# Kernel tuning notes

Measured on AMD Instinct MI355X. Metric: run time of the kernel, lower is better.

## Reference

```python
import jax, jax.numpy as jnp
import numpy as np
import math

B, T, C = 2, 2048, 1024
H = 16
D = C // H

def setup_inputs() -> dict:
    key = jax.random.key(0)
    k1, k2, k3, k4, k5 = jax.random.split(key, 5)
    scale = 0.02
    return {
        "x": jax.random.normal(k1, (B, T, C), dtype=jnp.float32),
        "w_attn": jax.random.normal(k2, (3 * C, C), dtype=jnp.float32) * scale,
        "b_attn": jax.random.normal(k3, (3 * C,), dtype=jnp.float32) * scale,
        "w_proj": jax.random.normal(k4, (C, C), dtype=jnp.float32) * scale,
        "b_proj": jax.random.normal(k5, (C,), dtype=jnp.float32) * scale,
    }

def reference(x, w_attn, b_attn, w_proj, b_proj):
    b, t, c = x.shape
    # c_attn: torch Linear -> x @ W.T + b, output [b, t, 3c]
    qkv = jnp.einsum('btc,fc->btf', x, w_attn) + b_attn
    # einops 'b t (a h d) -> a b h t d' with a=3, h=H
    qkv = qkv.reshape(b, t, 3, H, D).transpose(2, 0, 3, 1, 4)
    q, k, v = qkv[0], qkv[1], qkv[2]  # each [b, h, t, d]
    att = jnp.einsum('bhtd,bhsd->bhts', q, k) * (1.0 / math.sqrt(D))
    # causal mask: positions s > t are masked
    mask = jnp.tril(jnp.ones((t, t), dtype=bool))
    att = jnp.where(mask[None, None, :, :], att, jnp.float32(-jnp.inf))
    att = jax.nn.softmax(att, axis=-1)
    y = jnp.einsum('bhts,bhsd->bhtd', att, v)  # [b, h, t, d]
    y = y.transpose(0, 2, 1, 3).reshape(b, t, c)
    return jnp.einsum('btc,fc->btf', y, w_proj) + b_proj
```

## Files before the change

kernel.cpp:

```cpp
#include <hip/hip_runtime.h>
#include <hip/hip_bf16.h>
#include <stdint.h>

typedef unsigned short u16;
typedef __attribute__((ext_vector_type(8))) __bf16 bvec8;
typedef __attribute__((ext_vector_type(4))) float f32x4;
typedef __attribute__((ext_vector_type(16))) float f32x16;

__device__ __forceinline__ u16 f32_to_bf16(float f) {
    uint32_t u = __float_as_uint(f);
    u += 0x7fffu + ((u >> 16) & 1u);
    return (u16)(u >> 16);
}
__device__ __forceinline__ uint32_t pack_bf16x2(float lo, float hi) {
    union { __hip_bfloat162 h; uint32_t u; } c;
    c.h = __float22bfloat162_rn(make_float2(lo, hi));
    return c.u;
}

__device__ __forceinline__ void gl2lds16(const u16* g, u16* l) {
    void* gnc = const_cast<void*>((const void*)g);
    __builtin_amdgcn_global_load_lds(
        (__attribute__((address_space(1))) uint32_t*)gnc,
        (__attribute__((address_space(3))) uint32_t*)((void*)l),
        16, 0, 0);
}

__global__ __launch_bounds__(256) void cvt3(
    const float* __restrict__ a, int na4, const float* __restrict__ b, int nb4,
    const float* __restrict__ c, int nc4,
    u16* __restrict__ oa, u16* __restrict__ ob, u16* __restrict__ oc)
{
    int i = blockIdx.x * 256 + threadIdx.x;
    const float* src; u16* dst; int off;
    if (i < na4)             { src = a; dst = oa; off = i; }
    else if (i < na4 + nb4)  { src = b; dst = ob; off = i - na4; }
    else if (i < na4 + nb4 + nc4) { src = c; dst = oc; off = i - na4 - nb4; }
    else return;
    float4 v = ((const float4*)src)[off];
    ushort4 o;
    o.x = f32_to_bf16(v.x); o.y = f32_to_bf16(v.y);
    o.z = f32_to_bf16(v.z); o.w = f32_to_bf16(v.w);
    ((ushort4*)dst)[off] = o;
}

template <int BNt, bool OUT_BF16>
__global__ __launch_bounds__(256) void gemm_bt_bias(
    const u16* __restrict__ A, const u16* __restrict__ B,
    const float* __restrict__ bias, void* __restrict__ Cv,
    int M, int N, int K)
{
    constexpr int NT = BNt / 32;
    __shared__ __attribute__((aligned(16))) u16 As[128 * 32];
    __shared__ __attribute__((aligned(16))) u16 Bs[BNt * 32];

    const int tid = threadIdx.x, wave = tid >> 6, lane = tid & 63;
    const int col = lane & 15, quad = lane >> 4;
    const int m0 = blockIdx.y * 128, n0 = blockIdx.x * BNt;
    const int wm = (wave >> 1) * 64, wn = (wave & 1) * (BNt / 2);
    const int srow = lane >> 2, schunk = lane & 3;
    const u16* Ag = A + (size_t)(m0 + wave * 32) * K;

    f32x4 acc[4][NT];
#pragma unroll
    for (int i = 0; i < 4; i++)
#pragma unroll
        for (int j = 0; j < NT; j++) acc[i][j] = f32x4{0.f, 0.f, 0.f, 0.f};

    for (int k0 = 0; k0 < K; k0 += 32) {
        __syncthreads();
        gl2lds16(Ag + (size_t)(srow)      * K + k0 + schunk * 8, &As[(wave * 2 + 0) * 512]);
        gl2lds16(Ag + (size_t)(16 + srow) * K + k0 + schunk * 8, &As[(wave * 2 + 1) * 512]);
        if constexpr (BNt == 128) {
            const u16* Bg = B + (size_t)(n0 + wave * 32) * K;
            gl2lds16(Bg + (size_t)(srow)      * K + k0 + schunk * 8, &Bs[(wave * 2 + 0) * 512]);
            gl2lds16(Bg + (size_t)(16 + srow) * K + k0 + schunk * 8, &Bs[(wave * 2 + 1) * 512]);
        } else {
            const u16* Bg = B + (size_t)(n0 + wave * 16) * K;
            gl2lds16(Bg + (size_t)(srow)      * K + k0 + schunk * 8, &Bs[wave * 512]);
        }
        __syncthreads();

        bvec8 af[4], bfv[NT];
#pragma unroll
        for (int mt = 0; mt < 4; mt++)  af[mt]  = *(const bvec8*)&As[(wm + mt * 16 + col) * 32 + quad * 8];
#pragma unroll
        for (int nt = 0; nt < NT; nt++) bfv[nt] = *(const bvec8*)&Bs[(wn + nt * 16 + col) * 32 + quad * 8];
#pragma unroll
        for (int mt = 0; mt < 4; mt++)
#pragma unroll
            for (int nt = 0; nt < NT; nt++)
                acc[mt][nt] = __builtin_amdgcn_mfma_f32_16x16x32_bf16(af[mt], bfv[nt], acc[mt][nt], 0, 0, 0);
    }

#pragma unroll
    for (int mt = 0; mt < 4; mt++) {
#pragma unroll
        for (int r = 0; r < 4; r++) {
            const int m = m0 + wm + mt * 16 + quad * 4 + r;
#pragma unroll
            for (int nt = 0; nt < NT; nt++) {
                const int n = n0 + wn + nt * 16 + col;
                float v = acc[mt][nt][r] + bias[n];
                if (OUT_BF16) ((u16*)Cv)[(size_t)m * N + n] = f32_to_bf16(v);
                else          ((float*)Cv)[(size_t)m * N + n] = v;
            }
        }
    }
}

__global__ __launch_bounds__(256) void transpose_v(const u16* __restrict__ qkv,
                                                   u16* __restrict__ vT)
{
    __shared__ u16 Ts[64 * 74];
    const int tid = threadIdx.x;
    const int t0 = blockIdx.x * 64, h = blockIdx.y, b = blockIdx.z;
    const u16* src = qkv + (size_t)b * 2048 * 3072 + 2048 + h * 64;
#pragma unroll
    for (int k2 = 0; k2 < 2; k2++) {
        int c = k2 * 256 + tid, tl = c >> 3, ch = c & 7;
        *(uint4*)&Ts[tl * 74 + ch * 8] = *(const uint4*)(src + (size_t)(t0 + tl) * 3072 + ch * 8);
    }
    __syncthreads();
    u16* dst = vT + (size_t)((b * 16 + h) * 64) * 2048;
#pragma unroll
    for (int k2 = 0; k2 < 2; k2++) {
        int c = k2 * 256 + tid, d = c >> 3, tch = c & 7;
        u16 tmp[8];
#pragma unroll
        for (int j2 = 0; j2 < 8; j2++) {
            int p  = tch * 8 + j2;
            int sl = (p & 32) | ((p & 1) << 4) | ((p >> 1) & 15);
            tmp[j2] = Ts[sl * 74 + d];
        }
        *(uint4*)&dst[(size_t)d * 2048 + t0 + tch * 8] = *(const uint4*)tmp;
    }
}

__global__ __launch_bounds__(256) void attn_kernel(const u16* __restrict__ qkv,
                                                   const u16* __restrict__ vT,
                                                   u16* __restrict__ Y)
{
    __shared__ __attribute__((aligned(16))) u16 Qs[128 * 64];
    __shared__ __attribute__((aligned(16))) u16 Ks[2][64 * 64];
    __shared__ __attribute__((aligned(16))) u16 Vs[2][64 * 64];
    __shared__ __attribute__((aligned(16))) float Lbuf[4][32];

    const int tid = threadIdx.x, wave = tid >> 6, lane = tid & 63;
    const int l31 = lane & 31, hi = lane >> 5;

    const int g = blockIdx.x;
    const int b = g >> 4, h = g & 15;
    const int s_idx = blockIdx.y;

    const u16* qb = qkv + (size_t)b * 2048 * 3072;
    const u16* vb = vT + (size_t)g * 64 * 2048;

    const int c0 = wave * 64 + lane, c1 = 256 + c0;
    const int r0 = c0 >> 3, r1 = c1 >> 3;
    const int sw0 = ((c0 & 7) ^ (r0 & 7)) * 8, sw1 = ((c1 & 7) ^ (r1 & 7)) * 8;

#pragma unroll
    for (int phase = 0; phase < 2; ++phase) {
        const int qt = phase ? (15 - s_idx) : s_idx;
        const int q0 = qt * 128;
        const int nkt = 2 * qt + 2;

        __syncthreads();

#pragma unroll
        for (int g4 = 0; g4 < 4; g4++) {
            int c = g4 * 256 + wave * 64 + lane;
            int r = c >> 3, ch = c & 7;
            gl2lds16(qb + (size_t)(q0 + r) * 3072 + h * 64 + ((ch ^ (r & 7)) * 8),
                     &Qs[g4 * 2048 + wave * 512]);
        }
        gl2lds16(qb + (size_t)(r0) * 3072 + 1024 + h * 64 + sw0, &Ks[0][wave * 512]);
        gl2lds16(qb + (size_t)(r1) * 3072 + 1024 + h * 64 + sw1, &Ks[0][2048 + wave * 512]);
        gl2lds16(vb + (size_t)r0 * 2048 + sw0, &Vs[0][wave * 512]);
        gl2lds16(vb + (size_t)r1 * 2048 + sw1, &Vs[0][2048 + wave * 512]);
        asm volatile("s_waitcnt vmcnt(4)" ::: "memory");
        asm volatile("s_barrier" ::: "memory");

        const int q_lane = wave * 32 + l31;
        bvec8 qf[4];
#pragma unroll
        for (int c = 0; c < 4; c++)
            qf[c] = *(const bvec8*)&Qs[q_lane * 64 + (((c * 2 + hi) ^ (q_lane & 7)) * 8)];

        const int qmin  = q0 + wave * 32;
        const int qmax  = qmin + 31;
        const int q_act = qmin + l31;

        float l_acc = 0.f;
        f32x16 o0, o1;
#pragma unroll
        for (int i = 0; i < 16; i++) { o0[i] = 0.f; o1[i] = 0.f; }

        for (int kt = 0; kt < nkt; ++kt) {
            const int cur = kt & 1;
            if (kt + 1 < nkt) {
                const int s0n = (kt + 1) * 64, nb2 = cur ^ 1;
                gl2lds16(qb + (size_t)(s0n + r0) * 3072 + 1024 + h * 64 + sw0, &Ks[nb2][wave * 512]);
                gl2lds16(qb + (size_t)(s0n + r1) * 3072 + 1024 + h * 64 + sw1, &Ks[nb2][2048 + wave * 512]);
                gl2lds16(vb + (size_t)r0 * 2048 + s0n + sw0, &Vs[nb2][wave * 512]);
                gl2lds16(vb + (size_t)r1 * 2048 + s0n + sw1, &Vs[nb2][2048 + wave * 512]);
                asm volatile("s_waitcnt vmcnt(4)" ::: "memory");
            } else {
                asm volatile("s_waitcnt vmcnt(0)" ::: "memory");
            }
            asm volatile("s_barrier" ::: "memory");

            const int s_t0 = kt * 64;
            if (s_t0 <= qmax) {
                f32x16 sv0, sv1;
#pragma unroll
                for (int i = 0; i < 16; i++) { sv0[i] = 0.f; sv1[i] = 0.f; }
#pragma unroll
                for (int c = 0; c < 4; c++) {
                    bvec8 kf = *(const bvec8*)&Ks[cur][l31 * 64 + (((c * 2 + hi) ^ (l31 & 7)) * 8)];
                    sv0 = __builtin_amdgcn_mfma_f32_32x32x16_bf16(kf, qf[c], sv0, 0, 0, 0);
                }
#pragma unroll
                for (int c = 0; c < 4; c++) {
                    const int rr = 32 + l31;
                    bvec8 kf = *(const bvec8*)&Ks[cur][rr * 64 + (((c * 2 + hi) ^ (rr & 7)) * 8)];
                    sv1 = __builtin_amdgcn_mfma_f32_32x32x16_bf16(kf, qf[c], sv1, 0, 0, 0);
                }

                const bool msk = (s_t0 + 63 > qmin);
                float pv0[16], pv1[16];
#pragma unroll
                for (int i = 0; i < 16; i++) {
                    float p0 = __expf(sv0[i] * 0.125f);
                    float p1 = __expf(sv1[i] * 0.125f);
                    if (msk) {
                        const int srow = s_t0 + (i & 3) + 8 * (i >> 2) + 4 * hi;
                        if (srow > q_act)      p0 = 0.f;
                        if (srow + 32 > q_act) p1 = 0.f;
                    }
                    pv0[i] = p0; pv1[i] = p1;
                    l_acc += p0 + p1;
                }

                union { uint32_t u[4]; bvec8 v; } pf[4];
#pragma unroll
                for (int i2 = 0; i2 < 4; i2++) {
                    pf[0].u[i2] = pack_bf16x2(pv0[i2],     pv0[i2 + 8]);
                    pf[1].u[i2] = pack_bf16x2(pv0[i2 + 4], pv0[i2 + 12]);
                    pf[2].u[i2] = pack_bf16x2(pv1[i2],     pv1[i2 + 8]);
                    pf[3].u[i2] = pack_bf16x2(pv1[i2 + 4], pv1[i2 + 12]);
                }

#pragma unroll
                for (int jc = 0; jc < 4; jc++) {
                    const int lc = jc * 2 + hi;
                    bvec8 vf0 = *(const bvec8*)&Vs[cur][l31 * 64 + ((lc ^ (l31 & 7)) * 8)];
                    o0 = __builtin_amdgcn_mfma_f32_32x32x16_bf16(pf[jc].v, vf0, o0, 0, 0, 0);
                    const int rr = 32 + l31;
                    bvec8 vf1 = *(const bvec8*)&Vs[cur][rr * 64 + ((lc ^ (rr & 7)) * 8)];
                    o1 = __builtin_amdgcn_mfma_f32_32x32x16_bf16(pf[jc].v, vf1, o1, 0, 0, 0);
                }
            }
            asm volatile("s_barrier" ::: "memory");
        }

        l_acc += __shfl_xor(l_acc, 32);
        if (hi == 0) Lbuf[wave][l31] = l_acc;
        float inv[16];
#pragma unroll
        for (int g4 = 0; g4 < 4; g4++) {
            f32x4 lv = *(const f32x4*)&Lbuf[wave][g4 * 8 + 4 * hi];
#pragma unroll
            for (int jj = 0; jj < 4; jj++) inv[g4 * 4 + jj] = 1.0f / lv[jj];
        }
#pragma unroll
        for (int g4 = 0; g4 < 4; g4++) {
#pragma unroll
            for (int jj = 0; jj < 4; jj++) {
                const int i = g4 * 4 + jj;
                const int t = q0 + wave * 32 + g4 * 8 + 4 * hi + jj;
                u16* yrow = Y + (size_t)(b * 2048 + t) * 1024 + h * 64;
                yrow[l31]      = f32_to_bf16(o0[i] * inv[i]);
                yrow[32 + l31] = f32_to_bf16(o1[i] * inv[i]);
            }
        }
    }
}

extern "C" void kernel_launch(void* const* d_in, const int* in_sizes, int n_in,
                              void* d_out, int out_size, void* d_ws, size_t ws_size,
                              hipStream_t stream) {
    const float* x      = (const float*)d_in[0];
    const float* w_attn = (const float*)d_in[1];
    const float* b_attn = (const float*)d_in[2];
    const float* w_proj = (const float*)d_in[3];
    const float* b_proj = (const float*)d_in[4];
    float* out = (float*)d_out;

    u16* xb  = (u16*)d_ws;
    u16* wab = xb  + (size_t)4096 * 1024;
    u16* wpb = wab + (size_t)3072 * 1024;
    u16* qkv = wpb + (size_t)1024 * 1024;
    u16* y   = qkv + (size_t)4096 * 3072;
    u16* vT  = xb;

    const int na4 = 4096 * 1024 / 4, nb4 = 3072 * 1024 / 4, nc4 = 1024 * 1024 / 4;
    cvt3<<<(na4 + nb4 + nc4 + 255) / 256, 256, 0, stream>>>(
        x, na4, w_attn, nb4, w_proj, nc4, xb, wab, wpb);

    dim3 g1(3072 / 128, 4096 / 128);
    gemm_bt_bias<128, true><<<g1, 256, 0, stream>>>(xb, wab, b_attn, qkv, 4096, 3072, 1024);

    dim3 gt(32, 16, 2);
    transpose_v<<<gt, 256, 0, stream>>>(qkv, vT);

    dim3 g2(32, 8, 1);
    attn_kernel<<<g2, 256, 0, stream>>>(qkv, vT, y);

    dim3 g3(1024 / 64, 4096 / 128);
    gemm_bt_bias<64, false><<<g3, 256, 0, stream>>>(y, wpb, b_proj, out, 4096, 1024, 1024);
}
```

Baseline: 211.8 us.

## Split attention into single-wave blocks and fold softmax scale into QKV GEMM

The attention kernel changes from 256-thread blocks covering 128 queries to 64-thread single-wave blocks covering 32 queries. Each block processes a balanced pair of query tiles, which removes the block-wide barriers and gives four times as many blocks. Each wave now loads its own K/V tiles, so K/V traffic from global memory rises. Separately, the 1/sqrt(D) scale is applied to Q in the QKV GEMM epilogue instead of inside the exp loop, at the cost of one extra rounding of Q to bf16.

```diff
diff --git a/kernel.cpp b/kernel.cpp
--- a/kernel.cpp
+++ b/kernel.cpp
@@ -48,7 +48,7 @@
 __global__ __launch_bounds__(256) void gemm_bt_bias(
     const u16* __restrict__ A, const u16* __restrict__ B,
     const float* __restrict__ bias, void* __restrict__ Cv,
-    int M, int N, int K)
+    int M, int N, int K, int qncap)
 {
     constexpr int NT = BNt / 32;
     __shared__ __attribute__((aligned(16))) u16 As[128 * 32];
@@ -102,6 +102,7 @@
             for (int nt = 0; nt < NT; nt++) {
                 const int n = n0 + wn + nt * 16 + col;
                 float v = acc[mt][nt][r] + bias[n];
+                if (n < qncap) v *= 0.125f;
                 if (OUT_BF16) ((u16*)Cv)[(size_t)m * N + n] = f32_to_bf16(v);
                 else          ((float*)Cv)[(size_t)m * N + n] = v;
             }
@@ -137,60 +138,54 @@
     }
 }
 
-__global__ __launch_bounds__(256) void attn_kernel(const u16* __restrict__ qkv,
-                                                   const u16* __restrict__ vT,
-                                                   u16* __restrict__ Y)
+__global__ __launch_bounds__(64) void attn_kernel(const u16* __restrict__ qkv,
+                                                  const u16* __restrict__ vT,
+                                                  u16* __restrict__ Y)
 {
-    __shared__ __attribute__((aligned(16))) u16 Qs[128 * 64];
+    __shared__ __attribute__((aligned(16))) u16 Qs[32 * 64];
     __shared__ __attribute__((aligned(16))) u16 Ks[2][64 * 64];
     __shared__ __attribute__((aligned(16))) u16 Vs[2][64 * 64];
-    __shared__ __attribute__((aligned(16))) float Lbuf[4][32];
-
-    const int tid = threadIdx.x, wave = tid >> 6, lane = tid & 63;
+    __shared__ __attribute__((aligned(16))) float Lbuf[32];
+
+    const int lane = threadIdx.x & 63;
     const int l31 = lane & 31, hi = lane >> 5;
 
     const int g = blockIdx.x;
     const int b = g >> 4, h = g & 15;
-    const int s_idx = blockIdx.y;
+    const int pairIdx = blockIdx.y;
 
     const u16* qb = qkv + (size_t)b * 2048 * 3072;
     const u16* vb = vT + (size_t)g * 64 * 2048;
 
-    const int c0 = wave * 64 + lane, c1 = 256 + c0;
-    const int r0 = c0 >> 3, r1 = c1 >> 3;
-    const int sw0 = ((c0 & 7) ^ (r0 & 7)) * 8, sw1 = ((c1 & 7) ^ (r1 & 7)) * 8;
+    const int rl = lane >> 3;
+    const int sw = ((lane & 7) ^ rl) * 8;
+    const u16* kb = qb + 1024 + h * 64 + sw + (size_t)rl * 3072;
+    const u16* qbase = qb + h * 64 + sw + (size_t)rl * 3072;
+    const u16* vbl = vb + (size_t)rl * 2048 + sw;
 
 #pragma unroll
     for (int phase = 0; phase < 2; ++phase) {
-        const int qt = phase ? (15 - s_idx) : s_idx;
-        const int q0 = qt * 128;
-        const int nkt = 2 * qt + 2;
-
-        __syncthreads();
-
-#pragma unroll
-        for (int g4 = 0; g4 < 4; g4++) {
-            int c = g4 * 256 + wave * 64 + lane;
-            int r = c >> 3, ch = c & 7;
-            gl2lds16(qb + (size_t)(q0 + r) * 3072 + h * 64 + ((ch ^ (r & 7)) * 8),
-                     &Qs[g4 * 2048 + wave * 512]);
-        }
-        gl2lds16(qb + (size_t)(r0) * 3072 + 1024 + h * 64 + sw0, &Ks[0][wave * 512]);
-        gl2lds16(qb + (size_t)(r1) * 3072 + 1024 + h * 64 + sw1, &Ks[0][2048 + wave * 512]);
-        gl2lds16(vb + (size_t)r0 * 2048 + sw0, &Vs[0][wave * 512]);
-        gl2lds16(vb + (size_t)r1 * 2048 + sw1, &Vs[0][2048 + wave * 512]);
-        asm volatile("s_waitcnt vmcnt(4)" ::: "memory");
-        asm volatile("s_barrier" ::: "memory");
-
-        const int q_lane = wave * 32 + l31;
+        const int m = phase ? (63 - pairIdx) : pairIdx;
+        const int q0 = m * 32;
+        const int nkt = (m >> 1) + 1;
+
+#pragma unroll
+        for (int c = 0; c < 4; c++)
+            gl2lds16(qbase + (size_t)(q0 + c * 8) * 3072, &Qs[c * 512]);
+#pragma unroll
+        for (int c = 0; c < 8; c++)
+            gl2lds16(kb + (size_t)(c * 8) * 3072, &Ks[0][c * 512]);
+#pragma unroll
+        for (int c = 0; c < 8; c++)
+            gl2lds16(vbl + (size_t)(c * 8) * 2048, &Vs[0][c * 512]);
+        asm volatile("s_waitcnt vmcnt(16)" ::: "memory");
+
         bvec8 qf[4];
 #pragma unroll
         for (int c = 0; c < 4; c++)
-            qf[c] = *(const bvec8*)&Qs[q_lane * 64 + (((c * 2 + hi) ^ (q_lane & 7)) * 8)];
-
-        const int qmin  = q0 + wave * 32;
-        const int qmax  = qmin + 31;
-        const int q_act = qmin + l31;
+            qf[c] = *(const bvec8*)&Qs[l31 * 64 + (((c * 2 + hi) ^ (l31 & 7)) * 8)];
+
+        const int q_act = q0 + l31;
 
         float l_acc = 0.f;
         f32x16 o0, o1;
@@ -201,76 +196,74 @@
             const int cur = kt & 1;
             if (kt + 1 < nkt) {
                 const int s0n = (kt + 1) * 64, nb2 = cur ^ 1;
-                gl2lds16(qb + (size_t)(s0n + r0) * 3072 + 1024 + h * 64 + sw0, &Ks[nb2][wave * 512]);
-                gl2lds16(qb + (size_t)(s0n + r1) * 3072 + 1024 + h * 64 + sw1, &Ks[nb2][2048 + wave * 512]);
-                gl2lds16(vb + (size_t)r0 * 2048 + s0n + sw0, &Vs[nb2][wave * 512]);
-                gl2lds16(vb + (size_t)r1 * 2048 + s0n + sw1, &Vs[nb2][2048 + wave * 512]);
-                asm volatile("s_waitcnt vmcnt(4)" ::: "memory");
+#pragma unroll
+                for (int c = 0; c < 8; c++)
+                    gl2lds16(kb + (size_t)(s0n + c * 8) * 3072, &Ks[nb2][c * 512]);
+#pragma unroll
+                for (int c = 0; c < 8; c++)
+                    gl2lds16(vbl + (size_t)(c * 8) * 2048 + s0n, &Vs[nb2][c * 512]);
+                asm volatile("s_waitcnt vmcnt(16)" ::: "memory");
             } else {
                 asm volatile("s_waitcnt vmcnt(0)" ::: "memory");
             }
-            asm volatile("s_barrier" ::: "memory");
+
+            f32x16 sv0, sv1;
+#pragma unroll
+            for (int i = 0; i < 16; i++) { sv0[i] = 0.f; sv1[i] = 0.f; }
+#pragma unroll
+            for (int c = 0; c < 4; c++) {
+                bvec8 kf = *(const bvec8*)&Ks[cur][l31 * 64 + (((c * 2 + hi) ^ (l31 & 7)) * 8)];
+                sv0 = __builtin_amdgcn_mfma_f32_32x32x16_bf16(kf, qf[c], sv0, 0, 0, 0);
+            }
+#pragma unroll
+            for (int c = 0; c < 4; c++) {
+                const int rr = 32 + l31;
+                bvec8 kf = *(const bvec8*)&Ks[cur][rr * 64 + (((c * 2 + hi) ^ (rr & 7)) * 8)];
+                sv1 = __builtin_amdgcn_mfma_f32_32x32x16_bf16(kf, qf[c], sv1, 0, 0, 0);
+            }
 
             const int s_t0 = kt * 64;
-            if (s_t0 <= qmax) {
-                f32x16 sv0, sv1;
-#pragma unroll
-                for (int i = 0; i < 16; i++) { sv0[i] = 0.f; sv1[i] = 0.f; }
-#pragma unroll
-                for (int c = 0; c < 4; c++) {
-                    bvec8 kf = *(const bvec8*)&Ks[cur][l31 * 64 + (((c * 2 + hi) ^ (l31 & 7)) * 8)];
-                    sv0 = __builtin_amdgcn_mfma_f32_32x32x16_bf16(kf, qf[c], sv0, 0, 0, 0);
+            const bool msk = (s_t0 + 63 > q0);
+            float pv0[16], pv1[16];
+#pragma unroll
+            for (int i = 0; i < 16; i++) {
+                float p0 = __expf(sv0[i]);
+                float p1 = __expf(sv1[i]);
+                if (msk) {
+                    const int srow = s_t0 + (i & 3) + 8 * (i >> 2) + 4 * hi;
+                    if (srow > q_act)      p0 = 0.f;
+                    if (srow + 32 > q_act) p1 = 0.f;
                 }
-#pragma unroll
-                for (int c = 0; c < 4; c++) {
-                    const int rr = 32 + l31;
-                    bvec8 kf = *(const bvec8*)&Ks[cur][rr * 64 + (((c * 2 + hi) ^ (rr & 7)) * 8)];
-                    sv1 = __builtin_amdgcn_mfma_f32_32x32x16_bf16(kf, qf[c], sv1, 0, 0, 0);
-                }
-
-                const bool msk = (s_t0 + 63 > qmin);
-                float pv0[16], pv1[16];
-#pragma unroll
-                for (int i = 0; i < 16; i++) {
-                    float p0 = __expf(sv0[i] * 0.125f);
-                    float p1 = __expf(sv1[i] * 0.125f);
-                    if (msk) {
-                        const int srow = s_t0 + (i & 3) + 8 * (i >> 2) + 4 * hi;
-                        if (srow > q_act)      p0 = 0.f;
-                        if (srow + 32 > q_act) p1 = 0.f;
-                    }
-                    pv0[i] = p0; pv1[i] = p1;
-                    l_acc += p0 + p1;
-                }
-
-                union { uint32_t u[4]; bvec8 v; } pf[4];
-#pragma unroll
-                for (int i2 = 0; i2 < 4; i2++) {
-                    pf[0].u[i2] = pack_bf16x2(pv0[i2],     pv0[i2 + 8]);
-                    pf[1].u[i2] = pack_bf16x2(pv0[i2 + 4], pv0[i2 + 12]);
-                    pf[2].u[i2] = pack_bf16x2(pv1[i2],     pv1[i2 + 8]);
-                    pf[3].u[i2] = pack_bf16x2(pv1[i2 + 4], pv1[i2 + 12]);
-                }
-
-#pragma unroll
-                for (int jc = 0; jc < 4; jc++) {
-                    const int lc = jc * 2 + hi;
-                    bvec8 vf0 = *(const bvec8*)&Vs[cur][l31 * 64 + ((lc ^ (l31 & 7)) * 8)];
-                    o0 = __builtin_amdgcn_mfma_f32_32x32x16_bf16(pf[jc].v, vf0, o0, 0, 0, 0);
-                    const int rr = 32 + l31;
-                    bvec8 vf1 = *(const bvec8*)&Vs[cur][rr * 64 + ((lc ^ (rr & 7)) * 8)];
-                    o1 = __builtin_amdgcn_mfma_f32_32x32x16_bf16(pf[jc].v, vf1, o1, 0, 0, 0);
-                }
-            }
-            asm volatile("s_barrier" ::: "memory");
+                pv0[i] = p0; pv1[i] = p1;
+                l_acc += p0 + p1;
+            }
+
+            union { uint32_t u[4]; bvec8 v; } pf[4];
+#pragma unroll
+            for (int i2 = 0; i2 < 4; i2++) {
+                pf[0].u[i2] = pack_bf16x2(pv0[i2],     pv0[i2 + 8]);
+                pf[1].u[i2] = pack_bf16x2(pv0[i2 + 4], pv0[i2 + 12]);
+                pf[2].u[i2] = pack_bf16x2(pv1[i2],     pv1[i2 + 8]);
+                pf[3].u[i2] = pack_bf16x2(pv1[i2 + 4], pv1[i2 + 12]);
+            }
+
+#pragma unroll
+            for (int jc = 0; jc < 4; jc++) {
+                const int lc = jc * 2 + hi;
+                bvec8 vf0 = *(const bvec8*)&Vs[cur][l31 * 64 + ((lc ^ (l31 & 7)) * 8)];
+                o0 = __builtin_amdgcn_mfma_f32_32x32x16_bf16(pf[jc].v, vf0, o0, 0, 0, 0);
+                const int rr = 32 + l31;
+                bvec8 vf1 = *(const bvec8*)&Vs[cur][rr * 64 + ((lc ^ (rr & 7)) * 8)];
+                o1 = __builtin_amdgcn_mfma_f32_32x32x16_bf16(pf[jc].v, vf1, o1, 0, 0, 0);
+            }
         }
 
         l_acc += __shfl_xor(l_acc, 32);
-        if (hi == 0) Lbuf[wave][l31] = l_acc;
+        if (hi == 0) Lbuf[l31] = l_acc;
         float inv[16];
 #pragma unroll
         for (int g4 = 0; g4 < 4; g4++) {
-            f32x4 lv = *(const f32x4*)&Lbuf[wave][g4 * 8 + 4 * hi];
+            f32x4 lv = *(const f32x4*)&Lbuf[g4 * 8 + 4 * hi];
 #pragma unroll
             for (int jj = 0; jj < 4; jj++) inv[g4 * 4 + jj] = 1.0f / lv[jj];
         }
@@ -279,7 +272,7 @@
 #pragma unroll
             for (int jj = 0; jj < 4; jj++) {
                 const int i = g4 * 4 + jj;
-                const int t = q0 + wave * 32 + g4 * 8 + 4 * hi + jj;
+                const int t = q0 + g4 * 8 + 4 * hi + jj;
                 u16* yrow = Y + (size_t)(b * 2048 + t) * 1024 + h * 64;
                 yrow[l31]      = f32_to_bf16(o0[i] * inv[i]);
                 yrow[32 + l31] = f32_to_bf16(o1[i] * inv[i]);
@@ -310,14 +303,16 @@
         x, na4, w_attn, nb4, w_proj, nc4, xb, wab, wpb);
 
     dim3 g1(3072 / 128, 4096 / 128);
-    gemm_bt_bias<128, true><<<g1, 256, 0, stream>>>(xb, wab, b_attn, qkv, 4096, 3072, 1024);
+    gemm_bt_bias<128, true><<<g1, 256, 0, stream>>>(xb, wab, b_attn, qkv,
+                                                    4096, 3072, 1024, 1024);
 
     dim3 gt(32, 16, 2);
     transpose_v<<<gt, 256, 0, stream>>>(qkv, vT);
 
-    dim3 g2(32, 8, 1);
-    attn_kernel<<<g2, 256, 0, stream>>>(qkv, vT, y);
+    dim3 g2(32, 32, 1);
+    attn_kernel<<<g2, 64, 0, stream>>>(qkv, vT, y);
 
     dim3 g3(1024 / 64, 4096 / 128);
-    gemm_bt_bias<64, false><<<g3, 256, 0, stream>>>(y, wpb, b_proj, out, 4096, 1024, 1024);
-}
+    gemm_bt_bias<64, false><<<g3, 256, 0, stream>>>(y, wpb, b_proj, out,
+                                                    4096, 1024, 1024, 0);
+}
```

Result: slower. 219.6 us (+3.7%).
